# Kernel optimization log

Measured on AMD Instinct MI355X. Metric: run time of the kernel, lower is better.

## Reference

```python
import jax, jax.numpy as jnp
import numpy as np

PC_RANGE = (-140.8, -40.0, -3.0, 140.8, 40.0, 1.0)
VOX = (0.4, 0.4, 4.0)
H_GRID = 200   # (40 - (-40)) / 0.4
W_GRID = 704   # (140.8 - (-140.8)) / 0.4
C = 256        # embed_dim
N_BOX = 128
BN_EPS = 1e-5


def _make_boxes(key, n):
    # Realistic CCW-ordered 3D box corners (bottom 4 first, matching pred_box[:, :4, :2]).
    k1, k2, k3, k4, k5 = jax.random.split(key, 5)
    cx = jax.random.uniform(k1, (n,), minval=PC_RANGE[0] + 10.0, maxval=PC_RANGE[3] - 10.0)
    cy = jax.random.uniform(k2, (n,), minval=PC_RANGE[1] + 5.0, maxval=PC_RANGE[4] - 5.0)
    L = jax.random.uniform(k3, (n,), minval=2.0, maxval=8.0)
    Wd = jax.random.uniform(k4, (n,), minval=1.0, maxval=3.0)
    yaw = jax.random.uniform(k5, (n,), minval=0.0, maxval=2.0 * np.pi)
    # CCW offsets: (+l,+w), (-l,+w), (-l,-w), (+l,-w)
    ox = jnp.stack([L, -L, -L, L], axis=1) * 0.5   # [n,4]
    oy = jnp.stack([Wd, Wd, -Wd, -Wd], axis=1) * 0.5
    c, s = jnp.cos(yaw)[:, None], jnp.sin(yaw)[:, None]
    px = c * ox - s * oy + cx[:, None]
    py = s * ox + c * oy + cy[:, None]
    bot = jnp.stack([px, py, jnp.full_like(px, -1.0)], axis=-1)  # [n,4,3]
    top = jnp.stack([px, py, jnp.full_like(px, 1.0)], axis=-1)
    return jnp.concatenate([bot, top], axis=1)  # [n,8,3]


def setup_inputs() -> dict:
    key = jax.random.key(0)
    ks = jax.random.split(key, 16)
    inp = {
        "pred_box": _make_boxes(ks[0], N_BOX),
        "pred_score": jax.random.uniform(ks[1], (N_BOX,)),
        # MLP: Linear(25,C) -> ReLU -> Linear(C,C) -> ReLU -> Linear(C,C)
        "w1": jax.random.normal(ks[2], (25, C)) * 0.1,
        "b1": jnp.zeros((C,)),
        "w2": jax.random.normal(ks[3], (C, C)) * 0.05,
        "b2": jnp.zeros((C,)),
        "w3": jax.random.normal(ks[4], (C, C)) * 0.05,
        "b3": jnp.zeros((C,)),
        # 3 refine blocks x 2 convs, OIHW
        "conv_w": jax.random.normal(ks[5], (3, 2, C, C, 3, 3)) * 0.02,
        "bn_gamma": 1.0 + 0.1 * jax.random.normal(ks[6], (3, 2, C)),
        "bn_beta": 0.1 * jax.random.normal(ks[7], (3, 2, C)),
        "bn_mean": 0.1 * jax.random.normal(ks[8], (3, 2, C)),
        "bn_var": jax.random.uniform(ks[9], (3, 2, C), minval=0.5, maxval=1.5),
    }
    return inp


def _conv(x, w):
    return jax.lax.conv_general_dilated(
        x, w, window_strides=(1, 1), padding="SAME",
        dimension_numbers=("NCHW", "OIHW", "NCHW"))


def _bn(x, g, b, m, v):
    inv = g / jnp.sqrt(v + BN_EPS)
    return x * inv[None, :, None, None] + (b - m * inv)[None, :, None, None]


def reference(pred_box, pred_score, w1, b1, w2, b2, w3, b3,
              conv_w, bn_gamma, bn_beta, bn_mean, bn_var):
    n = pred_box.shape[0]
    # per-box feature: MLP(corners flattened + score) * score
    feat = jnp.concatenate([pred_box.reshape(n, -1), pred_score[:, None]], axis=1)  # [N,25]
    h = jax.nn.relu(feat @ w1 + b1)
    h = jax.nn.relu(h @ w2 + b2)
    obj = (h @ w3 + b3) * pred_score[:, None]  # [N,C]

    xmin, ymin = PC_RANGE[0], PC_RANGE[1]
    dx, dy = VOX[0], VOX[1]
    gx = (pred_box[:, :4, 0] - xmin) / dx  # [N,4] polygon verts in grid units
    gy = (pred_box[:, :4, 1] - ymin) / dy
    cxs = jnp.arange(W_GRID, dtype=pred_box.dtype) + 0.5  # cell centers
    cys = jnp.arange(H_GRID, dtype=pred_box.dtype) + 0.5

    # point-in-quad via 4 edge cross products (all >= 0 for CCW polygon)
    inside = jnp.ones((n, H_GRID, W_GRID), dtype=bool)
    for e in range(4):
        ax, ay = gx[:, e], gy[:, e]
        bx, by = gx[:, (e + 1) % 4], gy[:, (e + 1) % 4]
        vx, vy = bx - ax, by - ay
        c = (vx[:, None, None] * (cys[None, :, None] - ay[:, None, None])
             - vy[:, None, None] * (cxs[None, None, :] - ax[:, None, None]))  # [N,H,W]
        inside = inside & (c >= 0)
    insf = inside.astype(obj.dtype)

    feat_sum = jnp.einsum("nhw,nc->chw", insf, obj)        # masked scatter-add
    feat_cnt = jnp.maximum(insf.sum(axis=0), 1.0)           # [H,W]
    x = (feat_sum / feat_cnt[None])[None]                   # [1,C,H,W]

    for blk in range(3):
        res = x
        y = jax.nn.relu(_bn(_conv(x, conv_w[blk, 0]),
                            bn_gamma[blk, 0], bn_beta[blk, 0], bn_mean[blk, 0], bn_var[blk, 0]))
        y = _bn(_conv(y, conv_w[blk, 1]),
                bn_gamma[blk, 1], bn_beta[blk, 1], bn_mean[blk, 1], bn_var[blk, 1])
        x = jax.nn.relu(y + res)
    return x[0]  # [C,H,W]
```

## Files before the change

kernel.cpp:

```cpp
#include <hip/hip_runtime.h>

#define HG 200
#define WGR 704
#define CC 256
#define NBOX 128

typedef unsigned short u16;
typedef __attribute__((ext_vector_type(8))) short short8;
typedef __attribute__((ext_vector_type(4))) short short4v;
typedef __attribute__((ext_vector_type(4))) float floatx4;

typedef __attribute__((address_space(1))) const unsigned int guint;
typedef __attribute__((address_space(3))) unsigned int luint;

__device__ __forceinline__ float bf2f(u16 u) {
  unsigned int x = ((unsigned int)u) << 16;
  return __builtin_bit_cast(float, x);
}
__device__ __forceinline__ u16 f2bf(float f) {
  unsigned int x = __builtin_bit_cast(unsigned int, f);
  x += 0x7fffu + ((x >> 16) & 1u);
  return (u16)(x >> 16);
}

__global__ __launch_bounds__(256) void pack_w_kernel(const float* __restrict__ cw, u16* __restrict__ W2) {
  int i = blockIdx.x * 256 + threadIdx.x;
  int conv = i / 589824;
  int r = i - conv * 589824;
  int tap = r / 65536;
  int r2 = r - tap * 65536;
  int ck = r2 >> 13;
  int r3 = r2 & 8191;
  int cogrp = r3 >> 9;
  int r4 = r3 & 511;
  int lane = r4 >> 3;
  int j = r4 & 7;
  int co = cogrp * 16 + (lane & 15);
  int ci = ck * 32 + (lane >> 4) * 8 + j;
  W2[i] = f2bf(cw[((conv * 256 + co) * 256 + ci) * 9 + tap]);
}

__global__ __launch_bounds__(256) void bn_prep_kernel(const float* __restrict__ g, const float* __restrict__ b,
                                                      const float* __restrict__ m, const float* __restrict__ v,
                                                      float* __restrict__ binv, float* __restrict__ bbias) {
  int i = blockIdx.x * 256 + threadIdx.x;
  float inv = g[i] / sqrtf(v[i] + 1e-5f);
  binv[i] = inv;
  bbias[i] = b[i] - m[i] * inv;
}

__global__ __launch_bounds__(128) void box_prep_kernel(const float* __restrict__ pb, float* __restrict__ geo) {
  int b = threadIdx.x;
  float gx[4], gy[4];
#pragma unroll
  for (int j = 0; j < 4; ++j) {
    float px = pb[(b * 8 + j) * 3 + 0];
    float py = pb[(b * 8 + j) * 3 + 1];
    gx[j] = __fdiv_rn(__fsub_rn(px, -140.8f), 0.4f);
    gy[j] = __fdiv_rn(__fsub_rn(py, -40.0f), 0.4f);
  }
  float* g = geo + b * 16;
#pragma unroll
  for (int e = 0; e < 4; ++e) {
    g[e * 4 + 0] = gx[e];
    g[e * 4 + 1] = gy[e];
    g[e * 4 + 2] = __fsub_rn(gx[(e + 1) & 3], gx[e]);
    g[e * 4 + 3] = __fsub_rn(gy[(e + 1) & 3], gy[e]);
  }
}

__global__ __launch_bounds__(256) void mlp_kernel(
    const float* __restrict__ pb, const float* __restrict__ score,
    const float* __restrict__ w1, const float* __restrict__ b1,
    const float* __restrict__ w2, const float* __restrict__ b2,
    const float* __restrict__ w3, const float* __restrict__ b3,
    float* __restrict__ obj) {
  __shared__ float sf[25];
  __shared__ float h1[256];
  __shared__ float h2[256];
  int b = blockIdx.x, t = threadIdx.x;
  if (t < 24) sf[t] = pb[b * 24 + t];
  if (t == 24) sf[24] = score[b];
  __syncthreads();
  float a = b1[t];
  for (int k = 0; k < 25; ++k) a += sf[k] * w1[k * 256 + t];
  h1[t] = fmaxf(a, 0.0f);
  __syncthreads();
  a = b2[t];
  for (int k = 0; k < 256; ++k) a += h1[k] * w2[k * 256 + t];
  h2[t] = fmaxf(a, 0.0f);
  __syncthreads();
  a = b3[t];
  for (int k = 0; k < 256; ++k) a += h2[k] * w3[k * 256 + t];
  obj[b * 256 + t] = a * score[b];
}

__global__ __launch_bounds__(256) void raster_kernel(
    const float* __restrict__ geo, const float* __restrict__ obj, u16* __restrict__ x0) {
  __shared__ float sG[NBOX * 17];
  int tid = threadIdx.x;
  for (int i = tid; i < NBOX * 16; i += 256) sG[(i >> 4) * 17 + (i & 15)] = geo[i];
  __syncthreads();
  int wid = tid >> 6, lane = tid & 63;
  int cell = blockIdx.x * 4 + wid;
  int h = cell / WGR, w = cell - h * WGR;
  float cx = w + 0.5f, cy = h + 0.5f;

  auto test = [&](int n) -> bool {
    const float* g = &sG[n * 17];
    bool ok = true;
#pragma unroll
    for (int e = 0; e < 4; ++e) {
      float ax = g[e * 4 + 0], ay = g[e * 4 + 1];
      float vx = g[e * 4 + 2], vy = g[e * 4 + 3];
      float c = __fsub_rn(__fmul_rn(vx, __fsub_rn(cy, ay)),
                          __fmul_rn(vy, __fsub_rn(cx, ax)));
      ok = ok && (c >= 0.0f);
    }
    return ok;
  };

  unsigned long long m0 = __ballot(test(lane));
  unsigned long long m1 = __ballot(test(lane + 64));
  int cnt = __popcll(m0) + __popcll(m1);
  floatx4 s = {0.f, 0.f, 0.f, 0.f};
  while (m0) { int n = __builtin_ctzll(m0); m0 &= m0 - 1; s += *(const floatx4*)(obj + n * CC + lane * 4); }
  while (m1) { int n = 64 + __builtin_ctzll(m1); m1 &= m1 - 1; s += *(const floatx4*)(obj + n * CC + lane * 4); }
  float cf = fmaxf((float)cnt, 1.0f);
  short4v o;
#pragma unroll
  for (int j = 0; j < 4; ++j) o[j] = (short)f2bf(__fdiv_rn(s[j], cf));
  *(short4v*)(x0 + cell * CC + lane * 4) = o;
}

template <bool ADD_RES>
__global__ __launch_bounds__(256, 3) void conv_kernel(
    const u16* __restrict__ in, const u16* __restrict__ wgt,
    const float* __restrict__ bninv, const float* __restrict__ bnbias,
    const u16* __restrict__ res, u16* __restrict__ out) {
  __shared__ u16 sA[2 * 1056 * 8];

  const int w0 = blockIdx.x * 64;
  const int h0 = blockIdx.y * 2;
  const int c0g = blockIdx.z * 8;
  const int tid = threadIdx.x;
  const int lane = tid & 63;
  const int wid = tid >> 6;
  const int ln15 = lane & 15;
  const int quad = lane >> 4;
  const int mi = wid >> 1;
  const int ni = wid & 1;

  const u16* ga[5];
  bool gv[5];
#pragma unroll
  for (int j = 0; j < 5; ++j) {
    int I = wid + 4 * j;
    int s = I * 64 + lane;
    int r = s / 264;
    int rem = s - r * 264;
    int q = rem / 66;
    int px = rem - q * 66;
    int gh = h0 + r - 1;
    int gw = w0 + px - 1;
    bool ok = (I <= 16) && (s < 1056) &&
              ((unsigned)gh < (unsigned)HG) && ((unsigned)gw < (unsigned)WGR);
    ga[j] = in + (gh * WGR + gw) * CC + q * 8;
    gv[j] = ok;
    if (I <= 16 && s < 1056 && !ok) {
      short8 z = {};
      *(short8*)(&sA[s * 8]) = z;
      *(short8*)(&sA[(1056 + s) * 8]) = z;
    }
  }

  auto dma = [&](int buf) {
#pragma unroll
    for (int j = 0; j < 5; ++j) {
      int I = wid + 4 * j;
      if (I <= 16) {
        u16* lp = &sA[buf * 8448 + I * 512];
        if (gv[j])
          __builtin_amdgcn_global_load_lds((guint*)(const void*)ga[j], (luint*)(void*)lp, 16, 0, 0);
      }
      ga[j] += 32;
    }
  };

  const u16* wbase = wgt + ((size_t)(c0g + ni * 4)) * 512 + lane * 8;
  auto loadB = [&](int ck, int tap, short8* dst) {
#pragma unroll
    for (int nt = 0; nt < 4; ++nt)
      dst[nt] = *(const short8*)(wbase + ((tap * 8 + ck) * 16 + nt) * 512);
  };

  floatx4 acc[4][4] = {};
  short8 B[3][4];
  dma(0);

  for (int ck = 0; ck < 8; ++ck) {
    const int cur = ck & 1;
    __syncthreads();
    loadB(ck, 0, B[0]);
    loadB(ck, 1, B[1]);
    loadB(ck, 2, B[2]);
    if (ck < 7) dma(1 - cur);

    const u16* base = &sA[cur * 8448];
#pragma unroll
    for (int t = 0; t < 9; ++t) {
      const int kh = t / 3;
      const int kw = t - kh * 3;
      const short8* bc = B[t % 3];
#pragma unroll
      for (int mt = 0; mt < 4; ++mt) {
        const int r = mi + kh;
        const int px = mt * 16 + ln15 + kw;
        short8 af = *(const short8*)(base + ((r * 4 + quad) * 66 + px) * 8);
#pragma unroll
        for (int nt = 0; nt < 4; ++nt)
          acc[mt][nt] = __builtin_amdgcn_mfma_f32_16x16x32_bf16(af, bc[nt], acc[mt][nt], 0, 0, 0);
      }
      if (t + 3 < 9) loadB(ck, t + 3, B[t % 3]);
    }
  }

  const int h = h0 + mi;
  float binv[4], bbia[4];
#pragma unroll
  for (int nt = 0; nt < 4; ++nt) {
    int co = (c0g + ni * 4 + nt) * 16 + ln15;
    binv[nt] = bninv[co];
    bbia[nt] = bnbias[co];
  }

#pragma unroll
  for (int mt = 0; mt < 4; ++mt) {
#pragma unroll
    for (int nt = 0; nt < 4; ++nt) {
      int co = (c0g + ni * 4 + nt) * 16 + ln15;
#pragma unroll
      for (int r = 0; r < 4; ++r) {
        int w = w0 + mt * 16 + quad * 4 + r;
        int idx = (h * WGR + w) * CC + co;
        float v = acc[mt][nt][r] * binv[nt] + bbia[nt];
        if (ADD_RES) v += bf2f(res[idx]);
        v = fmaxf(v, 0.0f);
        out[idx] = f2bf(v);
      }
    }
  }
}

__global__ __launch_bounds__(256) void transpose_kernel(const u16* __restrict__ src, float* __restrict__ dst) {
  __shared__ u16 sT[64][68];
  int w0 = blockIdx.x * 64, h = blockIdx.y, c0 = blockIdx.z * 64;
  int tid = threadIdx.x;
  int cl = (tid & 15) * 4, wl = tid >> 4;
#pragma unroll
  for (int i = 0; i < 4; ++i) {
    int w = wl + i * 16;
    short4v v = *(const short4v*)(src + (h * WGR + w0 + w) * CC + c0 + cl);
    *(short4v*)(&sT[w][cl]) = v;
  }
  __syncthreads();
  int w4 = (tid & 15) * 4, ch = tid >> 4;
#pragma unroll
  for (int i = 0; i < 4; ++i) {
    int c = ch + i * 16;
    floatx4 v;
    v[0] = bf2f(sT[w4 + 0][c]);
    v[1] = bf2f(sT[w4 + 1][c]);
    v[2] = bf2f(sT[w4 + 2][c]);
    v[3] = bf2f(sT[w4 + 3][c]);
    *(floatx4*)(dst + (size_t)(c0 + c) * (HG * WGR) + h * WGR + w0 + w4) = v;
  }
}

extern "C" void kernel_launch(void* const* d_in, const int* in_sizes, int n_in,
                              void* d_out, int out_size, void* d_ws, size_t ws_size,
                              hipStream_t stream) {
  const float* pred_box = (const float*)d_in[0];
  const float* pred_score = (const float*)d_in[1];
  const float* w1 = (const float*)d_in[2];
  const float* b1 = (const float*)d_in[3];
  const float* w2 = (const float*)d_in[4];
  const float* b2 = (const float*)d_in[5];
  const float* w3 = (const float*)d_in[6];
  const float* b3 = (const float*)d_in[7];
  const float* conv_w = (const float*)d_in[8];
  const float* bng = (const float*)d_in[9];
  const float* bnb = (const float*)d_in[10];
  const float* bnm = (const float*)d_in[11];
  const float* bnv = (const float*)d_in[12];

  char* ws = (char*)d_ws;
  u16* W2       = (u16*)(ws);
  u16* Abuf     = (u16*)(ws + 7077888);
  float* obj    = (float*)(ws + 79167488);
  float* bninv  = (float*)(ws + 79298560);
  float* bnbias = (float*)(ws + 79304704);
  float* geo    = (float*)(ws + 79310848);
  u16* SCR = (u16*)d_out;
  float* OUT = (float*)d_out;

  pack_w_kernel<<<13824, 256, 0, stream>>>(conv_w, W2);
  bn_prep_kernel<<<6, 256, 0, stream>>>(bng, bnb, bnm, bnv, bninv, bnbias);
  box_prep_kernel<<<1, 128, 0, stream>>>(pred_box, geo);
  mlp_kernel<<<NBOX, 256, 0, stream>>>(pred_box, pred_score, w1, b1, w2, b2, w3, b3, obj);
  raster_kernel<<<35200, 256, 0, stream>>>(geo, obj, Abuf);

  dim3 cg(11, 100, 2);
  conv_kernel<false><<<cg, 256, 0, stream>>>(Abuf, W2 + 0 * 589824, bninv + 0 * 256, bnbias + 0 * 256, nullptr, SCR);
  conv_kernel<true ><<<cg, 256, 0, stream>>>(SCR,  W2 + 1 * 589824, bninv + 1 * 256, bnbias + 1 * 256, Abuf, Abuf);
  conv_kernel<false><<<cg, 256, 0, stream>>>(Abuf, W2 + 2 * 589824, bninv + 2 * 256, bnbias + 2 * 256, nullptr, SCR);
  conv_kernel<true ><<<cg, 256, 0, stream>>>(SCR,  W2 + 3 * 589824, bninv + 3 * 256, bnbias + 3 * 256, Abuf, Abuf);
  conv_kernel<false><<<cg, 256, 0, stream>>>(Abuf, W2 + 4 * 589824, bninv + 4 * 256, bnbias + 4 * 256, nullptr, SCR);
  conv_kernel<true ><<<cg, 256, 0, stream>>>(SCR,  W2 + 5 * 589824, bninv + 5 * 256, bnbias + 5 * 256, Abuf, Abuf);
  transpose_kernel<<<dim3(11, HG, 4), 256, 0, stream>>>(Abuf, OUT);
}
```

Baseline: 1.193 ms.

## Triple-buffer conv input tiles with vmcnt waits and zero-page padding loads

The conv kernel moves from a double-buffered LDS input tile with __syncthreads to a triple-buffered scheme. Prefetches run two chunks ahead, and a manual s_waitcnt vmcnt plus s_barrier replaces the full sync. Out-of-bounds padding now loads from a zeroed global page instead of branching and zero-filling LDS, so every thread issues uniform DMA and the vmcnt accounting stays exact. Weight loads for the next chunk are issued inside the current chunk's tap loop, BN params are loaded early, and MFMA bursts get s_setprio. This relies on a hand-counted vmcnt and on a zero page placed at a fixed offset inside the output buffer; it also raises LDS use, which could cost occupancy.

```diff
diff --git a/kernel.cpp b/kernel.cpp
--- a/kernel.cpp
+++ b/kernel.cpp
@@ -42,11 +42,13 @@
 
 __global__ __launch_bounds__(256) void bn_prep_kernel(const float* __restrict__ g, const float* __restrict__ b,
                                                       const float* __restrict__ m, const float* __restrict__ v,
-                                                      float* __restrict__ binv, float* __restrict__ bbias) {
+                                                      float* __restrict__ binv, float* __restrict__ bbias,
+                                                      float* __restrict__ zp) {
   int i = blockIdx.x * 256 + threadIdx.x;
   float inv = g[i] / sqrtf(v[i] + 1e-5f);
   binv[i] = inv;
   bbias[i] = b[i] - m[i] * inv;
+  if (blockIdx.x == 0 && threadIdx.x < 128) zp[threadIdx.x] = 0.0f;
 }
 
 __global__ __launch_bounds__(128) void box_prep_kernel(const float* __restrict__ pb, float* __restrict__ geo) {
@@ -137,8 +139,8 @@
 __global__ __launch_bounds__(256, 3) void conv_kernel(
     const u16* __restrict__ in, const u16* __restrict__ wgt,
     const float* __restrict__ bninv, const float* __restrict__ bnbias,
-    const u16* __restrict__ res, u16* __restrict__ out) {
-  __shared__ u16 sA[2 * 1056 * 8];
+    const u16* __restrict__ res, u16* __restrict__ out, const u16* __restrict__ zp) {
+  __shared__ u16 sA[3 * 1088 * 8];
 
   const int w0 = blockIdx.x * 64;
   const int h0 = blockIdx.y * 2;
@@ -151,11 +153,22 @@
   const int mi = wid >> 1;
   const int ni = wid & 1;
 
+  float binv[4], bbia[4];
+#pragma unroll
+  for (int nt = 0; nt < 4; ++nt) {
+    int co = (c0g + ni * 4 + nt) * 16 + ln15;
+    binv[nt] = bninv[co];
+    bbia[nt] = bnbias[co];
+  }
+  asm volatile("" ::: "memory");
+
   const u16* ga[5];
-  bool gv[5];
+  int ldsoff[5];
 #pragma unroll
   for (int j = 0; j < 5; ++j) {
     int I = wid + 4 * j;
+    if (I > 16) I = 16;
+    ldsoff[j] = I * 512;
     int s = I * 64 + lane;
     int r = s / 264;
     int rem = s - r * 264;
@@ -163,26 +176,15 @@
     int px = rem - q * 66;
     int gh = h0 + r - 1;
     int gw = w0 + px - 1;
-    bool ok = (I <= 16) && (s < 1056) &&
-              ((unsigned)gh < (unsigned)HG) && ((unsigned)gw < (unsigned)WGR);
-    ga[j] = in + (gh * WGR + gw) * CC + q * 8;
-    gv[j] = ok;
-    if (I <= 16 && s < 1056 && !ok) {
-      short8 z = {};
-      *(short8*)(&sA[s * 8]) = z;
-      *(short8*)(&sA[(1056 + s) * 8]) = z;
-    }
+    bool ok = (s < 1056) && ((unsigned)gh < (unsigned)HG) && ((unsigned)gw < (unsigned)WGR);
+    ga[j] = ok ? (in + (gh * WGR + gw) * CC + q * 8) : zp;
   }
 
   auto dma = [&](int buf) {
 #pragma unroll
     for (int j = 0; j < 5; ++j) {
-      int I = wid + 4 * j;
-      if (I <= 16) {
-        u16* lp = &sA[buf * 8448 + I * 512];
-        if (gv[j])
-          __builtin_amdgcn_global_load_lds((guint*)(const void*)ga[j], (luint*)(void*)lp, 16, 0, 0);
-      }
+      __builtin_amdgcn_global_load_lds((guint*)(const void*)ga[j],
+                                       (luint*)(void*)&sA[buf * 8704 + ldsoff[j]], 16, 0, 0);
       ga[j] += 32;
     }
   };
@@ -196,17 +198,22 @@
 
   floatx4 acc[4][4] = {};
   short8 B[3][4];
+
   dma(0);
-
+  asm volatile("" ::: "memory");
+  loadB(0, 0, B[0]);
+  loadB(0, 1, B[1]);
+  loadB(0, 2, B[2]);
+  asm volatile("" ::: "memory");
+  dma(1);
+  asm volatile("" ::: "memory");
+
+  int bs = 0;
   for (int ck = 0; ck < 8; ++ck) {
-    const int cur = ck & 1;
-    __syncthreads();
-    loadB(ck, 0, B[0]);
-    loadB(ck, 1, B[1]);
-    loadB(ck, 2, B[2]);
-    if (ck < 7) dma(1 - cur);
-
-    const u16* base = &sA[cur * 8448];
+    asm volatile("s_waitcnt vmcnt(17)" ::: "memory");
+    asm volatile("s_barrier" ::: "memory");
+
+    const u16* base = &sA[bs * 8704];
 #pragma unroll
     for (int t = 0; t < 9; ++t) {
       const int kh = t / 3;
@@ -217,23 +224,25 @@
         const int r = mi + kh;
         const int px = mt * 16 + ln15 + kw;
         short8 af = *(const short8*)(base + ((r * 4 + quad) * 66 + px) * 8);
+        __builtin_amdgcn_s_setprio(1);
 #pragma unroll
         for (int nt = 0; nt < 4; ++nt)
           acc[mt][nt] = __builtin_amdgcn_mfma_f32_16x16x32_bf16(af, bc[nt], acc[mt][nt], 0, 0, 0);
+        __builtin_amdgcn_s_setprio(0);
       }
-      if (t + 3 < 9) loadB(ck, t + 3, B[t % 3]);
-    }
+      if (t <= 5) loadB(ck, t + 3, B[t % 3]);
+      else if (ck < 7) loadB(ck + 1, t - 6, B[t % 3]);
+    }
+    asm volatile("" ::: "memory");
+    if (ck <= 5) {
+      int b2 = bs + 2; if (b2 >= 3) b2 -= 3;
+      dma(b2);
+    }
+    asm volatile("" ::: "memory");
+    bs = (bs == 2) ? 0 : bs + 1;
   }
 
   const int h = h0 + mi;
-  float binv[4], bbia[4];
-#pragma unroll
-  for (int nt = 0; nt < 4; ++nt) {
-    int co = (c0g + ni * 4 + nt) * 16 + ln15;
-    binv[nt] = bninv[co];
-    bbia[nt] = bnbias[co];
-  }
-
 #pragma unroll
   for (int mt = 0; mt < 4; ++mt) {
 #pragma unroll
@@ -303,19 +312,21 @@
   float* geo    = (float*)(ws + 79310848);
   u16* SCR = (u16*)d_out;
   float* OUT = (float*)d_out;
+  float* ZP = (float*)((char*)d_out + 120000000);
+  const u16* zp = (const u16*)ZP;
 
   pack_w_kernel<<<13824, 256, 0, stream>>>(conv_w, W2);
-  bn_prep_kernel<<<6, 256, 0, stream>>>(bng, bnb, bnm, bnv, bninv, bnbias);
+  bn_prep_kernel<<<6, 256, 0, stream>>>(bng, bnb, bnm, bnv, bninv, bnbias, ZP);
   box_prep_kernel<<<1, 128, 0, stream>>>(pred_box, geo);
   mlp_kernel<<<NBOX, 256, 0, stream>>>(pred_box, pred_score, w1, b1, w2, b2, w3, b3, obj);
   raster_kernel<<<35200, 256, 0, stream>>>(geo, obj, Abuf);
 
   dim3 cg(11, 100, 2);
-  conv_kernel<false><<<cg, 256, 0, stream>>>(Abuf, W2 + 0 * 589824, bninv + 0 * 256, bnbias + 0 * 256, nullptr, SCR);
-  conv_kernel<true ><<<cg, 256, 0, stream>>>(SCR,  W2 + 1 * 589824, bninv + 1 * 256, bnbias + 1 * 256, Abuf, Abuf);
-  conv_kernel<false><<<cg, 256, 0, stream>>>(Abuf, W2 + 2 * 589824, bninv + 2 * 256, bnbias + 2 * 256, nullptr, SCR);
-  conv_kernel<true ><<<cg, 256, 0, stream>>>(SCR,  W2 + 3 * 589824, bninv + 3 * 256, bnbias + 3 * 256, Abuf, Abuf);
-  conv_kernel<false><<<cg, 256, 0, stream>>>(Abuf, W2 + 4 * 589824, bninv + 4 * 256, bnbias + 4 * 256, nullptr, SCR);
-  conv_kernel<true ><<<cg, 256, 0, stream>>>(SCR,  W2 + 5 * 589824, bninv + 5 * 256, bnbias + 5 * 256, Abuf, Abuf);
+  conv_kernel<false><<<cg, 256, 0, stream>>>(Abuf, W2 + 0 * 589824, bninv + 0 * 256, bnbias + 0 * 256, nullptr, SCR, zp);
+  conv_kernel<true ><<<cg, 256, 0, stream>>>(SCR,  W2 + 1 * 589824, bninv + 1 * 256, bnbias + 1 * 256, Abuf, Abuf, zp);
+  conv_kernel<false><<<cg, 256, 0, stream>>>(Abuf, W2 + 2 * 589824, bninv + 2 * 256, bnbias + 2 * 256, nullptr, SCR, zp);
+  conv_kernel<true ><<<cg, 256, 0, stream>>>(SCR,  W2 + 3 * 589824, bninv + 3 * 256, bnbias + 3 * 256, Abuf, Abuf, zp);
+  conv_kernel<false><<<cg, 256, 0, stream>>>(Abuf, W2 + 4 * 589824, bninv + 4 * 256, bnbias + 4 * 256, nullptr, SCR, zp);
+  conv_kernel<true ><<<cg, 256, 0, stream>>>(SCR,  W2 + 5 * 589824, bninv + 5 * 256, bnbias + 5 * 256, Abuf, Abuf, zp);
   transpose_kernel<<<dim3(11, HG, 4), 256, 0, stream>>>(Abuf, OUT);
 }
```

Result: slower. 1.298 ms (+8.9%).
